# Kernel tuning notes

Measured on AMD Instinct MI355X. Metric: run time of the kernel, lower is better.

The kernel has to match this reference:

```python
import jax, jax.numpy as jnp
import numpy as np

B, N, C, H = 8, 4096, 1024, 16
D = C // H
SCALE = D ** -0.5

def setup_inputs() -> dict:
    key = jax.random.key(0)
    ks = jax.random.split(key, 6)
    s = C ** -0.5
    return {
        "fea": jax.random.normal(ks[0], (B, N, C), jnp.float32),
        "embedding": jax.random.normal(ks[1], (B, 1, C), jnp.float32),
        "Wq": jax.random.normal(ks[2], (C, C), jnp.float32) * s,
        "Wk": jax.random.normal(ks[3], (C, C), jnp.float32) * s,
        "Wv": jax.random.normal(ks[4], (C, C), jnp.float32) * s,
        "Wp": jax.random.normal(ks[5], (C, C), jnp.float32) * s,
        "bp": jnp.zeros((C,), jnp.float32),
    }

def reference(fea, embedding, Wq, Wk, Wv, Wp, bp):
    # q: [B,N,H,D]; k,v: [B,H,D] (kv seq len is 1)
    q = (fea @ Wq.T).reshape(B, N, H, D)
    k = (embedding @ Wk.T).reshape(B, H, D)
    v = (embedding @ Wv.T).reshape(B, H, D)
    # attn scores [B,N,H]: single-token key -> per-head dot product
    attn = jax.nn.sigmoid(jnp.einsum("bnhd,bhd->bnh", q, k) * SCALE)
    # broadcast-weight v over sequence: [B,N,H,D] -> [B,N,C]
    feat = (attn[..., None] * v[:, None, :, :]).reshape(B, N, C)
    feat = feat @ Wp.T + bp
    return feat + fea
```

## Files before the change

kernel.cpp:

```cpp
#include <hip/hip_runtime.h>
#include <hip/hip_bf16.h>
#include <stdint.h>

#define B 8
#define N 4096
#define C 1024
#define H 16
#define D 64

static __device__ __forceinline__ float bf_lo(uint32_t u) {
    union { uint32_t i; float f; } c; c.i = u << 16; return c.f;
}
static __device__ __forceinline__ float bf_hi(uint32_t u) {
    union { uint32_t i; float f; } c; c.i = u & 0xffff0000u; return c.f;
}

__global__ __launch_bounds__(256, 2)
void kv_kernel(const float* __restrict__ emb,
               const float* __restrict__ Wk,
               const float* __restrict__ Wv,
               float* __restrict__ kbuf,
               float* __restrict__ vbuf) {
    int wave = (blockIdx.x * blockDim.x + threadIdx.x) >> 6;
    int lane = threadIdx.x & 63;
    int r = wave;
    const float* Wrow = (r < C) ? (Wk + (size_t)r * C) : (Wv + (size_t)(r - C) * C);
    float4 w4[4];
#pragma unroll
    for (int j = 0; j < 4; ++j) w4[j] = *(const float4*)(Wrow + (lane + 64 * j) * 4);
    float acc[B];
#pragma unroll
    for (int b = 0; b < B; ++b) {
        const float* e = emb + (size_t)b * C;
        float a = 0.f;
#pragma unroll
        for (int j = 0; j < 4; ++j) {
            float4 e4 = *(const float4*)(e + (lane + 64 * j) * 4);
            a += w4[j].x * e4.x + w4[j].y * e4.y + w4[j].z * e4.z + w4[j].w * e4.w;
        }
        acc[b] = a;
    }
#pragma unroll
    for (int off = 32; off; off >>= 1)
#pragma unroll
        for (int b = 0; b < B; ++b) acc[b] += __shfl_xor(acc[b], off, 64);
    if (lane == 0) {
        float* dst = (r < C) ? (kbuf + r) : (vbuf + (r - C));
#pragma unroll
        for (int b = 0; b < B; ++b) dst[b * C] = acc[b];
    }
}

__global__ __launch_bounds__(256)
void wu_kernel(const float* __restrict__ Wq,
               const float* __restrict__ Wp,
               const float* __restrict__ kbuf,
               const float* __restrict__ vbuf,
               __hip_bfloat16* __restrict__ wbuf,
               __hip_bfloat16* __restrict__ ubuf) {
    int id = blockIdx.x;
    int t = threadIdx.x;
    if (id < 64) {
        int h = id >> 2;
        int c = ((id & 3) << 8) + t;
        const float* kk = kbuf + h * D;
        float acc[B];
#pragma unroll
        for (int b = 0; b < B; ++b) acc[b] = 0.f;
#pragma unroll 4
        for (int d = 0; d < D; ++d) {
            float wv = Wq[(size_t)(h * D + d) * C + c];
#pragma unroll
            for (int b = 0; b < B; ++b) acc[b] += kk[(size_t)b * C + d] * wv;
        }
#pragma unroll
        for (int b = 0; b < B; ++b)
            wbuf[(size_t)(b * H + h) * C + c] = __float2bfloat16(acc[b]);
    } else {
        int id2 = id - 64;
        int h = id2 >> 2;
        int cp = ((id2 & 3) << 8) + t;
        const float* vv = vbuf + h * D;
        float aq[4][B];
#pragma unroll
        for (int q = 0; q < 4; ++q)
#pragma unroll
            for (int b = 0; b < B; ++b) aq[q][b] = 0.f;
#pragma unroll
        for (int q = 0; q < 4; ++q) {
#pragma unroll
            for (int m = 0; m < 4; ++m) {
                int d0 = q * 16 + m * 4;
                float4 w4 = *(const float4*)(Wp + (size_t)cp * C + h * D + d0);
#pragma unroll
                for (int b = 0; b < B; ++b) {
                    const float* vb = vv + (size_t)b * C + d0;
                    aq[q][b] += w4.x * vb[0] + w4.y * vb[1]
                              + w4.z * vb[2] + w4.w * vb[3];
                }
            }
        }
#pragma unroll
        for (int b = 0; b < B; ++b)
            ubuf[(size_t)(b * H + h) * C + cp] =
                __float2bfloat16((aq[0][b] + aq[1][b]) + (aq[2][b] + aq[3][b]));
    }
}

__global__ __launch_bounds__(1024, 4)
void main_kernel(const float* __restrict__ fea,
                 const __hip_bfloat16* __restrict__ wbuf,
                 const __hip_bfloat16* __restrict__ ubuf,
                 const float* __restrict__ bp,
                 float* __restrict__ out) {
    __shared__ float w_f[H * C];
    __shared__ float u_f[H * C];
    const int b = blockIdx.y;
    const int tile = blockIdx.x;
    const int tid = threadIdx.x;

    {
        const uint32_t* wsrc = (const uint32_t*)(wbuf + (size_t)b * H * C);
        const uint32_t* usrc = (const uint32_t*)(ubuf + (size_t)b * H * C);
#pragma unroll
        for (int i = 0; i < H * C / 2 / 1024; ++i) {
            int wi = tid + i * 1024;
            uint32_t pw = wsrc[wi];
            uint32_t pu = usrc[wi];
            *(float2*)(w_f + 2 * wi) =
                make_float2(0.125f * bf_lo(pw), 0.125f * bf_hi(pw));
            *(float2*)(u_f + 2 * wi) = make_float2(bf_lo(pu), bf_hi(pu));
        }
    }
    __syncthreads();

    const int lane = tid & 63;
    const int wv = tid >> 6;
    const int row0 = tile * 128 + wv * 8;

    float4 bp4[4];
#pragma unroll
    for (int j = 0; j < 4; ++j) bp4[j] = *(const float4*)(bp + 4 * lane + 256 * j);

    const float* fbase = fea + ((size_t)b * N + row0) * C + 4 * lane;
    float* obase = out + ((size_t)b * N + row0) * C + 4 * lane;

#pragma unroll 1
    for (int g = 0; g < 4; ++g) {
        float4 f[2][4];
#pragma unroll
        for (int r = 0; r < 2; ++r)
#pragma unroll
            for (int j = 0; j < 4; ++j)
                f[r][j] = *(const float4*)(fbase + (size_t)(2 * g + r) * C + 256 * j);

        float4 acc[2][4];
#pragma unroll
        for (int r = 0; r < 2; ++r)
#pragma unroll
            for (int j = 0; j < 4; ++j) {
                acc[r][j].x = f[r][j].x + bp4[j].x;
                acc[r][j].y = f[r][j].y + bp4[j].y;
                acc[r][j].z = f[r][j].z + bp4[j].z;
                acc[r][j].w = f[r][j].w + bp4[j].w;
            }

#pragma unroll 1
        for (int h = 0; h < H; ++h) {
            const float* wrow = w_f + h * C + 4 * lane;
            float sp[2][4];
#pragma unroll
            for (int j = 0; j < 4; ++j) {
                float4 w4 = *(const float4*)(wrow + 256 * j);
#pragma unroll
                for (int r = 0; r < 2; ++r)
                    sp[r][j] = f[r][j].x * w4.x + f[r][j].y * w4.y
                             + f[r][j].z * w4.z + f[r][j].w * w4.w;
            }
            float s[2];
#pragma unroll
            for (int r = 0; r < 2; ++r)
                s[r] = (sp[r][0] + sp[r][1]) + (sp[r][2] + sp[r][3]);
#pragma unroll
            for (int off = 32; off; off >>= 1)
#pragma unroll
                for (int r = 0; r < 2; ++r) s[r] += __shfl_xor(s[r], off, 64);
#pragma unroll
            for (int r = 0; r < 2; ++r)
                s[r] = 1.f / (1.f + __expf(-s[r]));

            const float* urow = u_f + h * C + 4 * lane;
#pragma unroll
            for (int j = 0; j < 4; ++j) {
                float4 u4 = *(const float4*)(urow + 256 * j);
#pragma unroll
                for (int r = 0; r < 2; ++r) {
                    acc[r][j].x += s[r] * u4.x; acc[r][j].y += s[r] * u4.y;
                    acc[r][j].z += s[r] * u4.z; acc[r][j].w += s[r] * u4.w;
                }
            }
        }

#pragma unroll
        for (int r = 0; r < 2; ++r)
#pragma unroll
            for (int j = 0; j < 4; ++j)
                *(float4*)(obase + (size_t)(2 * g + r) * C + 256 * j) = acc[r][j];
    }
}

extern "C" void kernel_launch(void* const* d_in, const int* in_sizes, int n_in,
                              void* d_out, int out_size, void* d_ws, size_t ws_size,
                              hipStream_t stream) {
    const float* fea = (const float*)d_in[0];
    const float* emb = (const float*)d_in[1];
    const float* Wq  = (const float*)d_in[2];
    const float* Wk  = (const float*)d_in[3];
    const float* Wv  = (const float*)d_in[4];
    const float* Wp  = (const float*)d_in[5];
    const float* bp  = (const float*)d_in[6];
    float* out = (float*)d_out;

    char* ws = (char*)d_ws;
    float* kbuf = (float*)ws;
    float* vbuf = (float*)(ws + 32 * 1024);
    __hip_bfloat16* wbuf = (__hip_bfloat16*)(ws + 64 * 1024);
    __hip_bfloat16* ubuf = (__hip_bfloat16*)(ws + 320 * 1024);

    hipLaunchKernelGGL(kv_kernel, dim3(2 * C / 4), dim3(256), 0, stream,
                       emb, Wk, Wv, kbuf, vbuf);
    hipLaunchKernelGGL(wu_kernel, dim3(128), dim3(256), 0, stream,
                       Wq, Wp, kbuf, vbuf, wbuf, ubuf);
    hipLaunchKernelGGL(main_kernel, dim3(N / 128, B), dim3(1024), 0, stream,
                       fea, wbuf, ubuf, bp, out);
}
```

Measured before the change: 289.1 us.

## Use DPP wave reductions, four rows per pass, and split score/accumulate phases

```diff
diff --git a/kernel.cpp b/kernel.cpp
--- a/kernel.cpp
+++ b/kernel.cpp
@@ -13,6 +13,20 @@
 }
 static __device__ __forceinline__ float bf_hi(uint32_t u) {
     union { uint32_t i; float f; } c; c.i = u & 0xffff0000u; return c.f;
+}
+
+#define DPP_ADD(s, ctrl, rmask)                                              \
+    s += __int_as_float(__builtin_amdgcn_update_dpp(                         \
+        0, __float_as_int(s), ctrl, rmask, 0xf, true))
+
+static __device__ __forceinline__ float wave_sum_dpp(float s) {
+    DPP_ADD(s, 0x111, 0xf);
+    DPP_ADD(s, 0x112, 0xf);
+    DPP_ADD(s, 0x114, 0xf);
+    DPP_ADD(s, 0x118, 0xf);
+    DPP_ADD(s, 0x142, 0xa);
+    DPP_ADD(s, 0x143, 0xc);
+    return s;
 }
 
 __global__ __launch_bounds__(256, 2)
@@ -115,6 +129,7 @@
                  float* __restrict__ out) {
     __shared__ float w_f[H * C];
     __shared__ float u_f[H * C];
+    __shared__ float sig_s[16 * 64];
     const int b = blockIdx.y;
     const int tile = blockIdx.x;
     const int tid = threadIdx.x;
@@ -137,6 +152,7 @@
     const int lane = tid & 63;
     const int wv = tid >> 6;
     const int row0 = tile * 128 + wv * 8;
+    float* sigp = sig_s + wv * 64;
 
     float4 bp4[4];
 #pragma unroll
@@ -146,66 +162,72 @@
     float* obase = out + ((size_t)b * N + row0) * C + 4 * lane;
 
 #pragma unroll 1
-    for (int g = 0; g < 4; ++g) {
-        float4 f[2][4];
-#pragma unroll
-        for (int r = 0; r < 2; ++r)
+    for (int g = 0; g < 2; ++g) {
+        float4 f[4][4];
+#pragma unroll
+        for (int r = 0; r < 4; ++r)
 #pragma unroll
             for (int j = 0; j < 4; ++j)
-                f[r][j] = *(const float4*)(fbase + (size_t)(2 * g + r) * C + 256 * j);
-
-        float4 acc[2][4];
-#pragma unroll
-        for (int r = 0; r < 2; ++r)
-#pragma unroll
-            for (int j = 0; j < 4; ++j) {
-                acc[r][j].x = f[r][j].x + bp4[j].x;
-                acc[r][j].y = f[r][j].y + bp4[j].y;
-                acc[r][j].z = f[r][j].z + bp4[j].z;
-                acc[r][j].w = f[r][j].w + bp4[j].w;
-            }
+                f[r][j] = *(const float4*)(fbase + (size_t)(4 * g + r) * C + 256 * j);
 
 #pragma unroll 1
         for (int h = 0; h < H; ++h) {
             const float* wrow = w_f + h * C + 4 * lane;
-            float sp[2][4];
+            float4 w4[4];
+#pragma unroll
+            for (int j = 0; j < 4; ++j) w4[j] = *(const float4*)(wrow + 256 * j);
+            float s[4];
+#pragma unroll
+            for (int r = 0; r < 4; ++r) {
+                float a = f[r][0].x * w4[0].x + f[r][0].y * w4[0].y
+                        + f[r][0].z * w4[0].z + f[r][0].w * w4[0].w;
+                float c2 = f[r][1].x * w4[1].x + f[r][1].y * w4[1].y
+                         + f[r][1].z * w4[1].z + f[r][1].w * w4[1].w;
+                float d2 = f[r][2].x * w4[2].x + f[r][2].y * w4[2].y
+                         + f[r][2].z * w4[2].z + f[r][2].w * w4[2].w;
+                float e2 = f[r][3].x * w4[3].x + f[r][3].y * w4[3].y
+                         + f[r][3].z * w4[3].z + f[r][3].w * w4[3].w;
+                s[r] = (a + c2) + (d2 + e2);
+            }
+#pragma unroll
+            for (int r = 0; r < 4; ++r) s[r] = wave_sum_dpp(s[r]);
+#pragma unroll
+            for (int r = 0; r < 4; ++r) s[r] = __shfl(s[r], 63, 64);
+#pragma unroll
+            for (int r = 0; r < 4; ++r) s[r] = 1.f / (1.f + __expf(-s[r]));
+            if (lane == 0)
+                *(float4*)(sigp + h * 4) = make_float4(s[0], s[1], s[2], s[3]);
+        }
+
+#pragma unroll
+        for (int r = 0; r < 4; ++r)
 #pragma unroll
             for (int j = 0; j < 4; ++j) {
-                float4 w4 = *(const float4*)(wrow + 256 * j);
-#pragma unroll
-                for (int r = 0; r < 2; ++r)
-                    sp[r][j] = f[r][j].x * w4.x + f[r][j].y * w4.y
-                             + f[r][j].z * w4.z + f[r][j].w * w4.w;
-            }
-            float s[2];
-#pragma unroll
-            for (int r = 0; r < 2; ++r)
-                s[r] = (sp[r][0] + sp[r][1]) + (sp[r][2] + sp[r][3]);
-#pragma unroll
-            for (int off = 32; off; off >>= 1)
-#pragma unroll
-                for (int r = 0; r < 2; ++r) s[r] += __shfl_xor(s[r], off, 64);
-#pragma unroll
-            for (int r = 0; r < 2; ++r)
-                s[r] = 1.f / (1.f + __expf(-s[r]));
-
+                f[r][j].x += bp4[j].x; f[r][j].y += bp4[j].y;
+                f[r][j].z += bp4[j].z; f[r][j].w += bp4[j].w;
+            }
+
+#pragma unroll 1
+        for (int h = 0; h < H; ++h) {
+            float4 sg = *(const float4*)(sigp + h * 4);
+            float sgr[4] = {sg.x, sg.y, sg.z, sg.w};
             const float* urow = u_f + h * C + 4 * lane;
 #pragma unroll
             for (int j = 0; j < 4; ++j) {
                 float4 u4 = *(const float4*)(urow + 256 * j);
 #pragma unroll
-                for (int r = 0; r < 2; ++r) {
-                    acc[r][j].x += s[r] * u4.x; acc[r][j].y += s[r] * u4.y;
-                    acc[r][j].z += s[r] * u4.z; acc[r][j].w += s[r] * u4.w;
+                for (int r = 0; r < 4; ++r) {
+                    f[r][j].x += sgr[r] * u4.x; f[r][j].y += sgr[r] * u4.y;
+                    f[r][j].z += sgr[r] * u4.z; f[r][j].w += sgr[r] * u4.w;
                 }
             }
         }
 
 #pragma unroll
-        for (int r = 0; r < 2; ++r)
+        for (int r = 0; r < 4; ++r)
 #pragma unroll
             for (int j = 0; j < 4; ++j)
-                *(float4*)(obase + (size_t)(2 * g + r) * C + 256 * j) = acc[r][j];
+                *(float4*)(obase + (size_t)(4 * g + r) * C + 256 * j) = f[r][j];
     }
 }
 
```

Measured after the change: 280.8 us. -2.9%, faster.
